# Kernel tuning notes

Hardware: AMD Instinct MI355X
Metric: run time of the kernel (lower is better)

Reference implementation:

```python
import jax, jax.numpy as jnp
import numpy as np

N_NODES = 40000
N_EDGES = 640000
HIDDEN = 128


def setup_inputs() -> dict:
    key = jax.random.key(0)
    k1, k2, k3, k4 = jax.random.split(key, 4)
    x = jax.random.normal(k1, (N_NODES, HIDDEN), dtype=jnp.float32)
    edge_index = jax.random.randint(k2, (2, N_EDGES), 0, N_NODES, dtype=jnp.int64)
    # nn.Linear(2*hidden, 1): weight [1, 2*hidden], bias [1]
    bound = 1.0 / np.sqrt(2 * HIDDEN)
    att_w = jax.random.uniform(k3, (1, 2 * HIDDEN), minval=-bound, maxval=bound, dtype=jnp.float32)
    att_b = jax.random.uniform(k4, (1,), minval=-bound, maxval=bound, dtype=jnp.float32)
    eps = jnp.array([0.1], dtype=jnp.float32)
    return {"x": x, "edge_index": edge_index, "att_w": att_w, "att_b": att_b, "eps": eps}


def reference(x, edge_index, att_w, att_b, eps):
    d = x.shape[1]
    row, col = edge_index[0], edge_index[1]
    x_i = x[row]                               # [E, d]
    x_j = x[col]                               # [E, d]
    # att(cat([x_i, x_j])) == x_i @ w_i + x_j @ w_j + b  (avoids materializing concat)
    w = att_w[0]                               # [2d]
    logits = x_i @ w[:d] + x_j @ w[d:] + att_b[0]   # [E]
    alpha = jnp.tanh(logits)
    messages = alpha[:, None] * x_i            # [E, d]
    out = jax.ops.segment_sum(messages, col, num_segments=x.shape[0])  # scatter_add over col
    e = eps[0]
    return e * x + (1.0 - e) * out
```

## Files before the change

kernel.cpp:

```cpp
#include <hip/hip_runtime.h>
#include <hip/hip_fp16.h>
#include <math.h>


#define NHID 128
#define NNODES 40000
#define NEDGES 640000
#define CAP 64
#define CSTRIDE 16
#define POISON 0xAAAAAAAAu

typedef float    vfloat4 __attribute__((ext_vector_type(4)));
typedef unsigned vuint2  __attribute__((ext_vector_type(2)));
typedef unsigned vuint4  __attribute__((ext_vector_type(4)));

__device__ __forceinline__ float2 h2f2(unsigned u) {
    return __half22float2(__builtin_bit_cast(__half2, u));
}

__global__ __launch_bounds__(256) void pre_bucket_kernel(
    const float* __restrict__ x,
    const float* __restrict__ att_w,
    const float* __restrict__ att_b,
    const int* __restrict__ ei,
    float* __restrict__ s1,
    float* __restrict__ s2,
    __half* __restrict__ xh,
    unsigned* __restrict__ cursor,
    unsigned short* __restrict__ buck) {
    int g  = blockIdx.x / 3;
    int r3 = blockIdx.x % 3;
    if (r3 != 2) {
        int nb   = g * 2 + r3;
        int lane = threadIdx.x & 63;
        int half = lane >> 5;
        int sub  = lane & 31;
        int node = nb * 8 + (threadIdx.x >> 6) * 2 + half;

        vfloat4 xv = __builtin_nontemporal_load(
            (const vfloat4*)(x + (size_t)node * NHID) + sub);
        float4 w1 = ((const float4*)att_w)[sub];
        float4 w2 = ((const float4*)(att_w + NHID))[sub];

        __half2 h0; h0.x = __float2half_rn(xv.x); h0.y = __float2half_rn(xv.y);
        __half2 h1; h1.x = __float2half_rn(xv.z); h1.y = __float2half_rn(xv.w);
        vuint2 hu;
        hu.x = __builtin_bit_cast(unsigned, h0);
        hu.y = __builtin_bit_cast(unsigned, h1);
        __half* xp = xh + (size_t)(sub >> 4) * NNODES * 64 + (size_t)node * 64;
        __builtin_nontemporal_store(hu, (vuint2*)xp + (sub & 15));

        float p1 = xv.x * w1.x + xv.y * w1.y + xv.z * w1.z + xv.w * w1.w;
        float p2 = xv.x * w2.x + xv.y * w2.y + xv.z * w2.z + xv.w * w2.w;
#pragma unroll
        for (int off = 16; off > 0; off >>= 1) {
            p1 += __shfl_xor(p1, off, 64);
            p2 += __shfl_xor(p2, off, 64);
        }
        if (sub == 0) {
            s1[node] = p1;
            s2[node] = p2 + att_b[0];
        }
    } else {
        int e = g * 256 + threadIdx.x;
        int r = __builtin_nontemporal_load(ei + e);
        int c = __builtin_nontemporal_load(ei + NEDGES + e);
        unsigned old = atomicAdd(&cursor[c * CSTRIDE], 1u);
        int pos = (int)(old - POISON);
        if (pos >= 0 && pos < CAP) {
            buck[(size_t)c * CAP + pos] = (unsigned short)r;
        }
    }
}

__global__ __launch_bounds__(256) void gather_kernel(
    const __half* __restrict__ xh,
    const float* __restrict__ s1,
    const float* __restrict__ s2,
    const float* __restrict__ eps,
    const unsigned* __restrict__ cursor,
    const unsigned short* __restrict__ buck,
    float* __restrict__ out) {
    int plane = blockIdx.x & 1;
    int nb    = blockIdx.x >> 1;
    int lane  = threadIdx.x & 63;
    int k     = lane & 7;
    int hbase = lane & 56;
    int node  = nb * 32 + (threadIdx.x >> 6) * 8 + (lane >> 3);

    int cnt = (int)(__builtin_nontemporal_load(cursor + node * CSTRIDE) - POISON);
    cnt = (cnt < 0) ? 0 : ((cnt < CAP) ? cnt : CAP);

    float e = eps[0];
    float coef = 1.0f - e;
    float s2n = s2[node];

    vuint4 bv = __builtin_nontemporal_load(
        (const vuint4*)(buck + (size_t)node * CAP) + k);
    int   r_l[8];
    float a_l[8];
    {
        unsigned w[4] = {bv.x, bv.y, bv.z, bv.w};
#pragma unroll
        for (int t = 0; t < 8; t++) {
            int slot = 8 * k + t;
            int r = (int)((w[t >> 1] >> ((t & 1) * 16)) & 0xFFFFu);
            r_l[t] = (slot < cnt) ? r : 0;
            a_l[t] = (slot < cnt) ? coef * tanhf(s1[r_l[t]] + s2n) : 0.0f;
        }
    }

    const uint4* xp4 = (const uint4*)(xh + (size_t)plane * NNODES * 64);

    uint4 su = xp4[(size_t)node * 8 + k];
    float acc[8];
    {
        float2 f0 = h2f2(su.x), f1 = h2f2(su.y), f2 = h2f2(su.z), f3 = h2f2(su.w);
        acc[0] = e * f0.x; acc[1] = e * f0.y;
        acc[2] = e * f1.x; acc[3] = e * f1.y;
        acc[4] = e * f2.x; acc[5] = e * f2.y;
        acc[6] = e * f3.x; acc[7] = e * f3.y;
    }

#define SUBSEG(s)                                                           \
    {                                                                       \
        _Pragma("unroll")                                                   \
        for (int t = 0; t < 8; t++) {                                       \
            int   rj = __shfl(r_l[t], hbase | (s), 64);                     \
            float aj = __shfl(a_l[t], hbase | (s), 64);                     \
            uint4 v = xp4[(size_t)rj * 8 + k];                              \
            float2 g0 = h2f2(v.x), g1 = h2f2(v.y);                          \
            float2 g2 = h2f2(v.z), g3 = h2f2(v.w);                          \
            acc[0] += aj * g0.x; acc[1] += aj * g0.y;                       \
            acc[2] += aj * g1.x; acc[3] += aj * g1.y;                       \
            acc[4] += aj * g2.x; acc[5] += aj * g2.y;                       \
            acc[6] += aj * g3.x; acc[7] += aj * g3.y;                       \
        }                                                                   \
    }

    if (cnt > 0)  SUBSEG(0);
    if (cnt > 8)  SUBSEG(1);
    if (cnt > 16) SUBSEG(2);
    if (cnt > 24) SUBSEG(3);
    if (cnt > 32) SUBSEG(4);
    if (cnt > 40) SUBSEG(5);
    if (cnt > 48) SUBSEG(6);
    if (cnt > 56) SUBSEG(7);
#undef SUBSEG

    vfloat4* op = (vfloat4*)(out + (size_t)node * NHID + plane * 64 + k * 8);
    vfloat4 o0 = {acc[0], acc[1], acc[2], acc[3]};
    vfloat4 o1 = {acc[4], acc[5], acc[6], acc[7]};
    __builtin_nontemporal_store(o0, op);
    __builtin_nontemporal_store(o1, op + 1);
}

extern "C" void kernel_launch(void* const* d_in, const int* in_sizes, int n_in,
                              void* d_out, int out_size, void* d_ws, size_t ws_size,
                              hipStream_t stream) {
    const float* x     = (const float*)d_in[0];
    const int*   ei    = (const int*)d_in[1];
    const float* att_w = (const float*)d_in[2];
    const float* att_b = (const float*)d_in[3];
    const float* eps   = (const float*)d_in[4];
    float* out = (float*)d_out;

    float*          s1     = (float*)d_ws;
    float*          s2     = s1 + NNODES;
    __half*         xh     = (__half*)(s2 + NNODES);
    unsigned*       cursor = (unsigned*)(xh + (size_t)NNODES * NHID);
    unsigned short* buck   = (unsigned short*)(cursor + NNODES * CSTRIDE);

    pre_bucket_kernel<<<7500, 256, 0, stream>>>(
        x, att_w, att_b, ei, s1, s2, xh, cursor, buck);
    gather_kernel<<<2500, 256, 0, stream>>>(
        xh, s1, s2, eps, cursor, buck, out);
}
```

Baseline: 132.4 us.

## Precompute per-edge attention coefficients in a separate kernel before gather

Adds an alpha_kernel that computes coef*tanh(s1[row]+s2[col]) once per bucket slot with a fast exp-based tanh and stores it as fp16 next to the bucket indices. The gather kernel then loads packed (alpha, row) pairs and uses one shuffle per edge instead of two. Before, each plane block recomputed tanh and the s1 gathers, so that work was done twice. The cost is an extra launch, an extra bucket-sized array written and read, and alpha rounded to fp16.

```diff
diff --git a/kernel.cpp b/kernel.cpp
--- a/kernel.cpp
+++ b/kernel.cpp
@@ -73,13 +73,46 @@
     }
 }
 
-__global__ __launch_bounds__(256) void gather_kernel(
-    const __half* __restrict__ xh,
+__global__ __launch_bounds__(256) void alpha_kernel(
     const float* __restrict__ s1,
     const float* __restrict__ s2,
     const float* __restrict__ eps,
     const unsigned* __restrict__ cursor,
     const unsigned short* __restrict__ buck,
+    unsigned short* __restrict__ albk) {
+    int gid  = blockIdx.x * 256 + threadIdx.x;
+    int node = gid >> 5;
+    int j    = gid & 31;
+
+    int cnt = (int)(cursor[node * CSTRIDE] - POISON);
+    cnt = (cnt < 0) ? 0 : ((cnt < CAP) ? cnt : CAP);
+
+    unsigned pr = ((const unsigned*)(buck + (size_t)node * CAP))[j];
+    float coef = 1.0f - eps[0];
+    float s2n  = s2[node];
+
+    unsigned outp = 0;
+#pragma unroll
+    for (int h = 0; h < 2; h++) {
+        int slot = 2 * j + h;
+        int rid = (slot < cnt) ? (int)((pr >> (16 * h)) & 0xFFFFu) : 0;
+        float z  = s1[rid] + s2n;
+        float ez = __expf(2.0f * z);
+        float a  = coef * (1.0f - 2.0f / (ez + 1.0f));
+        unsigned ha = (unsigned)__builtin_bit_cast(
+            unsigned short, __float2half_rn(a));
+        if (slot >= cnt) ha = 0u;
+        outp |= ha << (16 * h);
+    }
+    __builtin_nontemporal_store(outp, (unsigned*)albk + gid);
+}
+
+__global__ __launch_bounds__(256) void gather_kernel(
+    const __half* __restrict__ xh,
+    const float* __restrict__ eps,
+    const unsigned* __restrict__ cursor,
+    const unsigned short* __restrict__ buck,
+    const unsigned short* __restrict__ albk,
     float* __restrict__ out) {
     int plane = blockIdx.x & 1;
     int nb    = blockIdx.x >> 1;
@@ -92,21 +125,21 @@
     cnt = (cnt < 0) ? 0 : ((cnt < CAP) ? cnt : CAP);
 
     float e = eps[0];
-    float coef = 1.0f - e;
-    float s2n = s2[node];
-
-    vuint4 bv = __builtin_nontemporal_load(
+
+    vuint4 rv = __builtin_nontemporal_load(
         (const vuint4*)(buck + (size_t)node * CAP) + k);
-    int   r_l[8];
-    float a_l[8];
+    vuint4 av = __builtin_nontemporal_load(
+        (const vuint4*)(albk + (size_t)node * CAP) + k);
+    unsigned c[8];
     {
-        unsigned w[4] = {bv.x, bv.y, bv.z, bv.w};
+        unsigned rw[4] = {rv.x, rv.y, rv.z, rv.w};
+        unsigned aw[4] = {av.x, av.y, av.z, av.w};
 #pragma unroll
         for (int t = 0; t < 8; t++) {
             int slot = 8 * k + t;
-            int r = (int)((w[t >> 1] >> ((t & 1) * 16)) & 0xFFFFu);
-            r_l[t] = (slot < cnt) ? r : 0;
-            a_l[t] = (slot < cnt) ? coef * tanhf(s1[r_l[t]] + s2n) : 0.0f;
+            unsigned rid = (rw[t >> 1] >> ((t & 1) * 16)) & 0xFFFFu;
+            unsigned ah  = (aw[t >> 1] >> ((t & 1) * 16)) & 0xFFFFu;
+            c[t] = (slot < cnt) ? ((ah << 16) | rid) : 0u;
         }
     }
 
@@ -126,8 +159,10 @@
     {                                                                       \
         _Pragma("unroll")                                                   \
         for (int t = 0; t < 8; t++) {                                       \
-            int   rj = __shfl(r_l[t], hbase | (s), 64);                     \
-            float aj = __shfl(a_l[t], hbase | (s), 64);                     \
+            unsigned ev = __shfl(c[t], hbase | (s), 64);                    \
+            int   rj = (int)(ev & 0xFFFFu);                                 \
+            float aj = __half2float(__builtin_bit_cast(                     \
+                __half, (unsigned short)(ev >> 16)));                       \
             uint4 v = xp4[(size_t)rj * 8 + k];                              \
             float2 g0 = h2f2(v.x), g1 = h2f2(v.y);                          \
             float2 g2 = h2f2(v.z), g3 = h2f2(v.w);                          \
@@ -170,9 +205,12 @@
     __half*         xh     = (__half*)(s2 + NNODES);
     unsigned*       cursor = (unsigned*)(xh + (size_t)NNODES * NHID);
     unsigned short* buck   = (unsigned short*)(cursor + NNODES * CSTRIDE);
+    unsigned short* albk   = buck + (size_t)NNODES * CAP;
 
     pre_bucket_kernel<<<7500, 256, 0, stream>>>(
         x, att_w, att_b, ei, s1, s2, xh, cursor, buck);
+    alpha_kernel<<<5000, 256, 0, stream>>>(
+        s1, s2, eps, cursor, buck, albk);
     gather_kernel<<<2500, 256, 0, stream>>>(
-        xh, s1, s2, eps, cursor, buck, out);
-}
+        xh, eps, cursor, buck, albk, out);
+}
```

After: 135.4 us. 2.2% more time.
